# Kernel tuning notes

Hardware: AMD Instinct MI355X
Metric: run time of the kernel (lower is better)

The kernel has to match this reference:

```python
import jax, jax.numpy as jnp
import numpy as np

N, M, D_K, D_V = 8192, 8192, 128, 128
SCALING = 1.0 / D_K  # module uses 1/d_k, NOT 1/sqrt(d_k)


def setup_inputs() -> dict:
    key = jax.random.key(0)
    kq, kk, kv = jax.random.split(key, 3)
    Q = jax.random.normal(kq, (N, D_K), dtype=jnp.float32)
    K = jax.random.normal(kk, (M, D_K), dtype=jnp.float32)
    V = jax.random.normal(kv, (M, D_V), dtype=jnp.float32)
    return {"Q": Q, "K": K, "V": V}


def reference(Q, K, V):
    # dots = Q @ K^T * (1/d_k)  -> [N, M]
    dots = jnp.einsum("nd,md->nm", Q, K) * SCALING
    # softmax over keys; dropout p=0 is identity
    attn = jax.nn.softmax(dots, axis=-1)
    # output = attn @ V -> [N, d_v]
    return jnp.einsum("nm,mv->nv", attn, V)
```

## Files before the change

### kernel.cpp

```cpp
#include <hip/hip_runtime.h>
#include <hip/hip_bf16.h>
#include <cstdint>
#include <cstddef>


typedef __attribute__((ext_vector_type(8))) short short8;
typedef __attribute__((ext_vector_type(4))) short shortx4;
typedef __attribute__((ext_vector_type(4))) float floatx4;
typedef __attribute__((ext_vector_type(16))) float floatx16;
typedef __attribute__((ext_vector_type(8))) _Float16 half8;

#define N_Q    8192
#define N_KV   8192
#define DHEAD  128
#define NSPLIT 8
#define BK     64
#define QSCALE (1.4426950408889634f / 128.0f)

static __device__ __forceinline__ unsigned short f2bf(float x) {
  __hip_bfloat16 h = __float2bfloat16(x);
  unsigned short u;
  __builtin_memcpy(&u, &h, 2);
  return u;
}

static __device__ __forceinline__ uint32_t pack_bf2(float a, float b) {
  return (uint32_t)f2bf(a) | ((uint32_t)f2bf(b) << 16);
}

#define MFMA32(a, b, c) __builtin_amdgcn_mfma_f32_32x32x16_bf16((a), (b), (c), 0, 0, 0)

#define GLD_LDS16(g, l)                                                        \
  __builtin_amdgcn_global_load_lds(                                            \
      (const __attribute__((address_space(1))) void*)(g),                      \
      (__attribute__((address_space(3))) void*)(l), 16, 0, 0)

__global__ void cvt_kernel(const float* __restrict__ K,
                           const float* __restrict__ V,
                           unsigned short* __restrict__ Kbc,
                           unsigned short* __restrict__ Vtc) {
  int bid = blockIdx.x;
  if (bid < 512) {
    int tid = bid * 256 + threadIdx.x;
    int ki = tid & 63;
    int ch = (tid >> 6) & 15;
    int b  = tid >> 10;
    const float* src = K + ((size_t)(b * 64 + ki) * DHEAD + ch * 8);
    floatx4 f0 = *(const floatx4*)src;
    floatx4 f1 = *(const floatx4*)(src + 4);
    short8 o;
    o[0] = (short)f2bf(f0[0]); o[1] = (short)f2bf(f0[1]);
    o[2] = (short)f2bf(f0[2]); o[3] = (short)f2bf(f0[3]);
    o[4] = (short)f2bf(f1[0]); o[5] = (short)f2bf(f1[1]);
    o[6] = (short)f2bf(f1[2]); o[7] = (short)f2bf(f1[3]);
    *(short8*)(Kbc + (size_t)tid * 8) = o;
  } else {
    int tid = (bid - 512) * 256 + threadIdx.x;
    int kh = tid & 1;
    int dv = (tid >> 1) & 127;
    int c2 = (tid >> 8) & 7;
    int b  = tid >> 11;
    int k0 = b * 64 + c2 * 8 + kh * 4;
    shortx4 o;
    o[0] = (short)f2bf(V[(size_t)(k0 + 0) * DHEAD + dv]);
    o[1] = (short)f2bf(V[(size_t)(k0 + 1) * DHEAD + dv]);
    o[2] = (short)f2bf(V[(size_t)(k0 + 2) * DHEAD + dv]);
    o[3] = (short)f2bf(V[(size_t)(k0 + 3) * DHEAD + dv]);
    *(shortx4*)(Vtc + (size_t)tid * 4) = o;
  }
}

__global__ __launch_bounds__(256, 2) void attn_kernel(
    const float* __restrict__ Q, const unsigned short* __restrict__ Kbc,
    const unsigned short* __restrict__ Vtc, _Float16* __restrict__ Opart,
    float* __restrict__ Lst) {
  __shared__ unsigned short lds[8192 + 8192 + 4 * 2048];
  unsigned short* Ks  = lds;
  unsigned short* Vts = lds + 8192;
  unsigned short* Pa  = lds + 16384 + (threadIdx.x >> 6) * 2048;

  const int t = threadIdx.x;
  const int w = t >> 6;
  const int lane = t & 63;
  const int h = lane >> 5;
  const int c = lane & 31;
  const int qbase = blockIdx.x * 128 + w * 32;
  const int sp = blockIdx.y;

  short8 qf[8];
  {
    const float* qrow = Q + (size_t)(qbase + c) * DHEAD + h * 8;
#pragma unroll
    for (int dc = 0; dc < 8; ++dc) {
      floatx4 f0 = *(const floatx4*)(qrow + dc * 16);
      floatx4 f1 = *(const floatx4*)(qrow + dc * 16 + 4);
      short8 s;
      s[0] = (short)f2bf(f0[0] * QSCALE); s[1] = (short)f2bf(f0[1] * QSCALE);
      s[2] = (short)f2bf(f0[2] * QSCALE); s[3] = (short)f2bf(f0[3] * QSCALE);
      s[4] = (short)f2bf(f1[0] * QSCALE); s[5] = (short)f2bf(f1[1] * QSCALE);
      s[6] = (short)f2bf(f1[2] * QSCALE); s[7] = (short)f2bf(f1[3] * QSCALE);
      qf[dc] = s;
    }
  }

  floatx16 acc[4];
#pragma unroll
  for (int i = 0; i < 4; ++i)
#pragma unroll
    for (int r = 0; r < 16; ++r) acc[i][r] = 0.f;
  float lsum = 0.f;

  const int NT = N_KV / NSPLIT / BK;
  const int kb0 = sp * NT;

  for (int it = 0; it < NT; ++it) {
    const int kb = kb0 + it;
    {
      const unsigned short* kg = Kbc + (size_t)kb * 8192;
      const unsigned short* vg = Vtc + (size_t)kb * 8192;
#pragma unroll
      for (int i = 0; i < 4; ++i) {
        int slab = w * 4 + i;
        GLD_LDS16(kg + slab * 512 + lane * 8, Ks + slab * 512);
        GLD_LDS16(vg + slab * 512 + lane * 8, Vts + slab * 512);
      }
    }
    __syncthreads();

    const short8* KsF = (const short8*)Ks;
    uint32_t* pa32 = (uint32_t*)Pa;
#pragma unroll
    for (int st = 0; st < 2; ++st) {
      floatx16 sc;
#pragma unroll
      for (int r = 0; r < 16; ++r) sc[r] = 0.f;
#pragma unroll
      for (int dc = 0; dc < 8; ++dc) {
        short8 a = KsF[(dc * 2 + h) * 64 + st * 32 + c];
        sc = MFMA32(a, qf[dc], sc);
      }
#pragma unroll
      for (int r2 = 0; r2 < 4; ++r2) {
        float p0 = exp2f(sc[r2 * 4 + 0]);
        float p1 = exp2f(sc[r2 * 4 + 1]);
        float p2 = exp2f(sc[r2 * 4 + 2]);
        float p3 = exp2f(sc[r2 * 4 + 3]);
        lsum += (p0 + p1) + (p2 + p3);
        int di = ((st * 4 + r2) * 32 + c) * 4 + h * 2;
        pa32[di + 0] = pack_bf2(p0, p1);
        pa32[di + 1] = pack_bf2(p2, p3);
      }
    }

    const short8* PaF = (const short8*)Pa;
    const short8* VtsF = (const short8*)Vts;
#pragma unroll
    for (int kc = 0; kc < 4; ++kc) {
      short8 pf = PaF[(kc * 2 + h) * 32 + c];
#pragma unroll
      for (int nb = 0; nb < 4; ++nb) {
        short8 bv = VtsF[(kc * 2 + h) * 128 + nb * 32 + c];
        acc[nb] = MFMA32(pf, bv, acc[nb]);
      }
    }
    __syncthreads();
  }

  lsum += __shfl_xor(lsum, 32, 64);
  if (h == 0) Lst[(size_t)sp * N_Q + qbase + c] = lsum;
  _Float16* op = Opart + ((size_t)sp * N_Q + qbase) * DHEAD;
#pragma unroll
  for (int nb = 0; nb < 4; ++nb)
#pragma unroll
    for (int r = 0; r < 16; ++r) {
      int row = (r & 3) + 8 * (r >> 2) + 4 * h;
      op[(size_t)row * DHEAD + nb * 32 + c] = (_Float16)acc[nb][r];
    }
}

__global__ void merge_kernel(const _Float16* __restrict__ Opart,
                             const float* __restrict__ Lst,
                             float* __restrict__ out) {
  int tid = blockIdx.x * blockDim.x + threadIdx.x;
  int g = tid >> 4;
  int d0 = (tid & 15) * 8;
  float den = 0.f;
  float num[8] = {0.f, 0.f, 0.f, 0.f, 0.f, 0.f, 0.f, 0.f};
#pragma unroll
  for (int s = 0; s < NSPLIT; ++s) {
    den += Lst[(size_t)s * N_Q + g];
    half8 o = *(const half8*)(Opart + ((size_t)s * N_Q + g) * DHEAD + d0);
#pragma unroll
    for (int j = 0; j < 8; ++j) num[j] += (float)o[j];
  }
  float inv = 1.0f / den;
  floatx4 r0 = (floatx4){num[0] * inv, num[1] * inv, num[2] * inv, num[3] * inv};
  floatx4 r1 = (floatx4){num[4] * inv, num[5] * inv, num[6] * inv, num[7] * inv};
  float* dst = out + (size_t)g * DHEAD + d0;
  *(floatx4*)dst = r0;
  *(floatx4*)(dst + 4) = r1;
}

extern "C" void kernel_launch(void* const* d_in, const int* in_sizes, int n_in,
                              void* d_out, int out_size, void* d_ws,
                              size_t ws_size, hipStream_t stream) {
  const float* Q = (const float*)d_in[0];
  const float* K = (const float*)d_in[1];
  const float* V = (const float*)d_in[2];
  float* out = (float*)d_out;

  char* ws = (char*)d_ws;
  unsigned short* Kbc = (unsigned short*)(ws);
  unsigned short* Vtc = (unsigned short*)(ws + (2u << 20));
  _Float16* Opart = (_Float16*)(ws + (4u << 20));
  float* Lst = (float*)(ws + (20u << 20));

  cvt_kernel<<<dim3(1536), dim3(256), 0, stream>>>(K, V, Kbc, Vtc);
  attn_kernel<<<dim3(N_Q / 128, NSPLIT), dim3(256), 0, stream>>>(Q, Kbc, Vtc,
                                                                 Opart, Lst);
  merge_kernel<<<dim3(512), dim3(256), 0, stream>>>(Opart, Lst, out);
}
```

Measured before the change: 114.9 us.

## Double-buffer K/V in LDS and keep P in registers via permlane swap

Splits LDS into two K/V stages and prefetches the next block while the current one is computed, removing the load-then-barrier stall at each iteration start. The softmax probabilities are packed with v_cvt_pk_bf16_f32 and rearranged across half-waves with permlane32_swap, so they feed the PV MFMA directly instead of going through an LDS scratch buffer. It also uses the raw exp2 builtin and raises wave priority around the MFMA sections. The risk is that correctness depends on the compiler-inserted wait before the barrier covering the async global-to-LDS loads, and that the permlane layout must match the MFMA operand layout.

```diff
diff --git a/kernel.cpp b/kernel.cpp
--- a/kernel.cpp
+++ b/kernel.cpp
@@ -24,8 +24,10 @@
   return u;
 }
 
-static __device__ __forceinline__ uint32_t pack_bf2(float a, float b) {
-  return (uint32_t)f2bf(a) | ((uint32_t)f2bf(b) << 16);
+static __device__ __forceinline__ uint32_t cvt_pk_bf16(float lo, float hi) {
+  uint32_t r;
+  asm("v_cvt_pk_bf16_f32 %0, %1, %2" : "=v"(r) : "v"(lo), "v"(hi));
+  return r;
 }
 
 #define MFMA32(a, b, c) __builtin_amdgcn_mfma_f32_32x32x16_bf16((a), (b), (c), 0, 0, 0)
@@ -74,10 +76,7 @@
     const float* __restrict__ Q, const unsigned short* __restrict__ Kbc,
     const unsigned short* __restrict__ Vtc, _Float16* __restrict__ Opart,
     float* __restrict__ Lst) {
-  __shared__ unsigned short lds[8192 + 8192 + 4 * 2048];
-  unsigned short* Ks  = lds;
-  unsigned short* Vts = lds + 8192;
-  unsigned short* Pa  = lds + 16384 + (threadIdx.x >> 6) * 2048;
+  __shared__ unsigned short lds[2 * 16384];
 
   const int t = threadIdx.x;
   const int w = t >> 6;
@@ -113,54 +112,70 @@
   const int NT = N_KV / NSPLIT / BK;
   const int kb0 = sp * NT;
 
+  auto stage = [&](unsigned short* dstK, int kb) {
+    const unsigned short* kg = Kbc + (size_t)kb * 8192;
+    const unsigned short* vg = Vtc + (size_t)kb * 8192;
+#pragma unroll
+    for (int i = 0; i < 4; ++i) {
+      int slab = w * 4 + i;
+      GLD_LDS16(kg + slab * 512 + lane * 8, dstK + slab * 512);
+      GLD_LDS16(vg + slab * 512 + lane * 8, dstK + 8192 + slab * 512);
+    }
+  };
+
+  stage(lds, kb0);
+  __syncthreads();
+
   for (int it = 0; it < NT; ++it) {
-    const int kb = kb0 + it;
-    {
-      const unsigned short* kg = Kbc + (size_t)kb * 8192;
-      const unsigned short* vg = Vtc + (size_t)kb * 8192;
-#pragma unroll
-      for (int i = 0; i < 4; ++i) {
-        int slab = w * 4 + i;
-        GLD_LDS16(kg + slab * 512 + lane * 8, Ks + slab * 512);
-        GLD_LDS16(vg + slab * 512 + lane * 8, Vts + slab * 512);
-      }
-    }
-    __syncthreads();
-
-    const short8* KsF = (const short8*)Ks;
-    uint32_t* pa32 = (uint32_t*)Pa;
+    const int cur = it & 1;
+    if (it + 1 < NT) stage(lds + (cur ^ 1) * 16384, kb0 + it + 1);
+
+    const short8* KsF  = (const short8*)(lds + cur * 16384);
+    const short8* VtsF = (const short8*)(lds + cur * 16384 + 8192);
+
 #pragma unroll
     for (int st = 0; st < 2; ++st) {
       floatx16 sc;
 #pragma unroll
       for (int r = 0; r < 16; ++r) sc[r] = 0.f;
+      __builtin_amdgcn_s_setprio(1);
 #pragma unroll
       for (int dc = 0; dc < 8; ++dc) {
         short8 a = KsF[(dc * 2 + h) * 64 + st * 32 + c];
         sc = MFMA32(a, qf[dc], sc);
       }
-#pragma unroll
-      for (int r2 = 0; r2 < 4; ++r2) {
-        float p0 = exp2f(sc[r2 * 4 + 0]);
-        float p1 = exp2f(sc[r2 * 4 + 1]);
-        float p2 = exp2f(sc[r2 * 4 + 2]);
-        float p3 = exp2f(sc[r2 * 4 + 3]);
-        lsum += (p0 + p1) + (p2 + p3);
-        int di = ((st * 4 + r2) * 32 + c) * 4 + h * 2;
-        pa32[di + 0] = pack_bf2(p0, p1);
-        pa32[di + 1] = pack_bf2(p2, p3);
-      }
-    }
-
-    const short8* PaF = (const short8*)Pa;
-    const short8* VtsF = (const short8*)Vts;
-#pragma unroll
-    for (int kc = 0; kc < 4; ++kc) {
-      short8 pf = PaF[(kc * 2 + h) * 32 + c];
-#pragma unroll
-      for (int nb = 0; nb < 4; ++nb) {
-        short8 bv = VtsF[(kc * 2 + h) * 128 + nb * 32 + c];
-        acc[nb] = MFMA32(pf, bv, acc[nb]);
+      __builtin_amdgcn_s_setprio(0);
+
+      float p[16];
+#pragma unroll
+      for (int r = 0; r < 16; ++r) p[r] = __builtin_amdgcn_exp2f(sc[r]);
+      lsum += ((((p[0] + p[1]) + (p[2] + p[3])) +
+                ((p[4] + p[5]) + (p[6] + p[7]))) +
+               (((p[8] + p[9]) + (p[10] + p[11])) +
+                ((p[12] + p[13]) + (p[14] + p[15]))));
+
+#pragma unroll
+      for (int kc2 = 0; kc2 < 2; ++kc2) {
+        const int g = kc2 * 8;
+        uint32_t x0 = cvt_pk_bf16(p[g + 0], p[g + 1]);
+        uint32_t x1 = cvt_pk_bf16(p[g + 2], p[g + 3]);
+        uint32_t y0 = cvt_pk_bf16(p[g + 4], p[g + 5]);
+        uint32_t y1 = cvt_pk_bf16(p[g + 6], p[g + 7]);
+        auto s0 = __builtin_amdgcn_permlane32_swap(x0, y0, false, false);
+        auto s1 = __builtin_amdgcn_permlane32_swap(x1, y1, false, false);
+        union { uint32_t u[4]; short8 s; } pu;
+        pu.u[0] = s0[0];
+        pu.u[1] = s1[0];
+        pu.u[2] = s0[1];
+        pu.u[3] = s1[1];
+        const int kc = st * 2 + kc2;
+        __builtin_amdgcn_s_setprio(1);
+#pragma unroll
+        for (int nb = 0; nb < 4; ++nb) {
+          short8 bv = VtsF[(kc * 2 + h) * 128 + nb * 32 + c];
+          acc[nb] = MFMA32(pu.s, bv, acc[nb]);
+        }
+        __builtin_amdgcn_s_setprio(0);
       }
     }
     __syncthreads();
```

Result: faster. 106.0 us (-7.7%).
